# Kernel tuning notes

Hardware: AMD Instinct MI355X
Metric: run time of the kernel (lower is better)

## Reference

```python
import jax, jax.numpy as jnp
from jax import lax
import numpy as np

RANK = 4
C_IN = 32
C_OUT = 64
H, W = 128, 256
L1 = (H + 2, W + 2)      # conv k=3, pad=2, stride=1 -> H+2
L2 = (L1[0] + 2, L1[1] + 2)
EPS = 1e-5


def setup_inputs() -> dict:
    key = jax.random.key(0)
    ks = jax.random.split(key, 12)
    s = lambda k, shp: jax.random.normal(k, shp, dtype=jnp.float32) * 0.05
    inp = {
        "x": jax.random.normal(ks[0], (16, C_IN, H, W), dtype=jnp.float32),
        # layer 1: rank basis kernels, bias, outer combining-weight logits
        "w1": s(ks[1], (RANK, C_OUT, C_IN, 3, 3)),
        "b1": jnp.zeros((C_OUT,), jnp.float32),
        "a1h": s(ks[2], (RANK, L1[0])),
        "a1w": s(ks[3], (RANK, L1[1])),
        "g1": jnp.ones((C_OUT,), jnp.float32),
        "be1": jnp.zeros((C_OUT,), jnp.float32),
        # layer 2
        "w2": s(ks[4], (RANK, C_OUT, C_OUT, 3, 3)),
        "b2": jnp.zeros((C_OUT,), jnp.float32),
        "a2h": s(ks[5], (RANK, L2[0])),
        "a2w": s(ks[6], (RANK, L2[1])),
        "g2": jnp.ones((C_OUT,), jnp.float32),
        "be2": jnp.zeros((C_OUT,), jnp.float32),
    }
    return inp


def _combining_weights(ah, aw):
    # outer sum of row/col logits, softmax over rank -> [rank, Lh, Lw]
    return jax.nn.softmax(ah[:, :, None] + aw[:, None, :], axis=0)


def _lrlc(x, w, b, cw):
    # x: [B, Cin, H, W]; w: [rank, Cout, Cin, 3, 3]; cw: [rank, H', W']
    rank, co, ci, kh, kw = w.shape
    y = lax.conv_general_dilated(
        x, w.reshape(rank * co, ci, kh, kw),
        window_strides=(1, 1), padding=[(2, 2), (2, 2)],
        dimension_numbers=("NCHW", "OIHW", "NCHW"))
    B, _, Ho, Wo = y.shape
    y = y.reshape(B, rank, co, Ho, Wo)
    return jnp.einsum("brohw,rhw->bohw", y, cw) + b[None, :, None, None]


def _bn_relu(x, g, be):
    # training-mode BatchNorm2d (batch stats, biased variance) + ReLU
    mean = jnp.mean(x, axis=(0, 2, 3), keepdims=True)
    var = jnp.var(x, axis=(0, 2, 3), keepdims=True)
    xn = (x - mean) * lax.rsqrt(var + EPS)
    return jax.nn.relu(xn * g[None, :, None, None] + be[None, :, None, None])


def _maxpool3(x):
    return lax.reduce_window(x, -jnp.inf, lax.max,
                             (1, 1, 3, 3), (1, 1, 3, 3), "VALID")


def reference(x, w1, b1, a1h, a1w, g1, be1, w2, b2, a2h, a2w, g2, be2):
    cw1 = _combining_weights(a1h, a1w)
    h = _lrlc(x, w1, b1, cw1)
    h = _bn_relu(h, g1, be1)
    cw2 = _combining_weights(a2h, a2w)
    h = _lrlc(h, w2, b2, cw2)
    h = _bn_relu(h, g2, be2)
    return _maxpool3(h)
```

## Files before the change

kernel.cpp:

```cpp
#include <hip/hip_runtime.h>
#include <hip/hip_bf16.h>
#include <math.h>

#define COUT 64
#define EPS  1e-5f

typedef __hip_bfloat16 bf16;
typedef short  short8  __attribute__((ext_vector_type(8)));
typedef short  short4v __attribute__((ext_vector_type(4)));
typedef float  floatx4 __attribute__((ext_vector_type(4)));

__device__ __forceinline__ short bf16_bits(float f) {
    union { __hip_bfloat16 h; short s; } u;
    u.h = __float2bfloat16(f);
    return u.s;
}
__device__ __forceinline__ float bits_to_f32(short s) {
    union { __hip_bfloat16 h; short s; } u;
    u.s = s;
    return __bfloat162float(u.h);
}

#define NV1   33800
#define NV2   34584
#define XPAD_PLANE  (132*260)
#define H1_PLANE    (134*262)
#define H2_PLANE    (132*260)
#define NPOS1 (16*130*258)
#define NPOS2 (16*132*260)

__global__ void zero_f_kernel(float* __restrict__ p, int n) {
    int i = blockIdx.x*blockDim.x + threadIdx.x;
    if (i < n) p[i] = 0.f;
}
__global__ void zero4_kernel(uint4* __restrict__ p, long n4) {
    long i = (long)blockIdx.x*blockDim.x + threadIdx.x;
    for (; i < n4; i += (long)gridDim.x*blockDim.x) p[i] = make_uint4(0,0,0,0);
}

__global__ void cwv_kernel(const float* __restrict__ ah, const float* __restrict__ aw,
                           float* __restrict__ cwv, int Nv, int Wv, int Lh, int Lw) {
    int idx = blockIdx.x*blockDim.x + threadIdx.x;
    if (idx >= Nv) return;
    int oh = idx / Wv, ow = idx - oh*Wv;
    if (ow > Lw-1) ow = Lw-1;
    float v0 = ah[0*Lh+oh] + aw[0*Lw+ow];
    float v1 = ah[1*Lh+oh] + aw[1*Lw+ow];
    float v2 = ah[2*Lh+oh] + aw[2*Lw+ow];
    float v3 = ah[3*Lh+oh] + aw[3*Lw+ow];
    float m = fmaxf(fmaxf(v0,v1), fmaxf(v2,v3));
    v0 = __expf(v0-m); v1 = __expf(v1-m); v2 = __expf(v2-m); v3 = __expf(v3-m);
    float inv = 1.f/(v0+v1+v2+v3);
    cwv[0*(size_t)Nv+idx] = v0*inv; cwv[1*(size_t)Nv+idx] = v1*inv;
    cwv[2*(size_t)Nv+idx] = v2*inv; cwv[3*(size_t)Nv+idx] = v3*inv;
}

template<int CIN_, int NSLICES>
__global__ void pack_kernel(const float* __restrict__ w, short* __restrict__ Apk) {
    int gid = blockIdx.x*256 + threadIdx.x;
    if (gid >= NSLICES*1024) return;
    int l = gid & 63, t = (gid >> 6) & 15, s = gid >> 10;
    int m = t*16 + (l & 15);
    int r = m >> 6, co = m & 63;
    int kbase = s*32 + ((l >> 4) << 3);
    short8 v;
    #pragma unroll
    for (int j = 0; j < 8; ++j) {
        int k = kbase + j;
        int tap = k / CIN_, ci = k % CIN_;
        v[j] = bf16_bits(w[(((size_t)(r*COUT + co))*CIN_ + ci)*9 + tap]);
    }
    *reinterpret_cast<short8*>(Apk + (size_t)gid*8) = v;
}

__global__ void xpad_kernel(const float* __restrict__ x, short* __restrict__ xp) {
    int row = blockIdx.x;
    int b = row / 132, ih = row - b*132;
    int ci = threadIdx.x & 31, iw0 = threadIdx.x >> 5;
    for (int iw = iw0; iw < 260; iw += 8) {
        float v = 0.f;
        if (ih >= 2 && ih < 130 && iw >= 2 && iw < 258)
            v = x[(((size_t)b*32 + ci)*128 + (ih-2))*256 + (iw-2)];
        xp[((size_t)row*260 + iw)*32 + ci] = bf16_bits(v);
    }
}

template<int CIN_, int NSLICES>
__launch_bounds__(256, 2)
__global__ void lrlc_conv(const short* __restrict__ Bpl, const short* __restrict__ Apk,
                          const float* __restrict__ cwv, const float* __restrict__ bias,
                          short* __restrict__ Out, float* __restrict__ sum, float* __restrict__ sq,
                          int Wv, int Hout, int Wreal, int Nv, int inPlanePos,
                          int outW, int outPlanePos, int outPad) {
    const int tid  = threadIdx.x;
    const int w    = tid >> 6, l = tid & 63;
    const int quad = l >> 4, l15 = l & 15;
    const int b    = blockIdx.y;
    const int n0   = blockIdx.x * 128;

    __shared__ float cwS[4*128];
    for (int t = tid; t < 512; t += 256) {
        int r = t >> 7, nn = t & 127;
        int n = n0 + nn; if (n > Nv-1) n = Nv-1;
        cwS[t] = cwv[(size_t)r*Nv + n];
    }
    __syncthreads();

    const short* Bb = Bpl + (size_t)b*inPlanePos*CIN_;
    int bOff[8];
    #pragma unroll
    for (int j = 0; j < 8; ++j) bOff[j] = (n0 + j*16 + l15)*CIN_ + quad*8;
    const short* Aw = Apk + (size_t)(w*64 + l)*8;

    floatx4 acc[4][8];
    #pragma unroll
    for (int i = 0; i < 4; ++i)
        #pragma unroll
        for (int j = 0; j < 8; ++j)
            acc[i][j] = (floatx4){0.f,0.f,0.f,0.f};

    #pragma unroll
    for (int s = 0; s < NSLICES; ++s) {
        const int tap = (CIN_ == 32) ? s : (s >> 1);
        const int cb  = (CIN_ == 32) ? 0 : ((s & 1) << 5);
        const int koff = ((tap/3)*Wv + (tap%3))*CIN_ + cb;
        short8 bfr[8], afr[4];
        #pragma unroll
        for (int j = 0; j < 8; ++j)
            bfr[j] = *reinterpret_cast<const short8*>(Bb + bOff[j] + koff);
        #pragma unroll
        for (int i = 0; i < 4; ++i)
            afr[i] = *reinterpret_cast<const short8*>(Aw + (size_t)(s*16 + i*4)*512);
        #pragma unroll
        for (int i = 0; i < 4; ++i)
            #pragma unroll
            for (int j = 0; j < 8; ++j)
                acc[i][j] = __builtin_amdgcn_mfma_f32_16x16x32_bf16(afr[i], bfr[j], acc[i][j], 0, 0, 0);
    }

    const int co_base = w*16 + quad*4;
    float bs[4];
    #pragma unroll
    for (int rg = 0; rg < 4; ++rg) bs[rg] = bias[co_base + rg];
    float st[4] = {0.f,0.f,0.f,0.f}, st2[4] = {0.f,0.f,0.f,0.f};
    #pragma unroll
    for (int j = 0; j < 8; ++j) {
        int nl = j*16 + l15;
        int n  = n0 + nl;
        int oh = n / Wv, ow = n - oh*Wv;
        bool valid = (ow < Wreal) && (oh < Hout);
        float c0 = cwS[nl], c1 = cwS[128+nl], c2 = cwS[256+nl], c3 = cwS[384+nl];
        short4v pk;
        #pragma unroll
        for (int rg = 0; rg < 4; ++rg) {
            float v = acc[0][j][rg]*c0 + acc[1][j][rg]*c1
                    + acc[2][j][rg]*c2 + acc[3][j][rg]*c3 + bs[rg];
            if (valid) { st[rg] += v; st2[rg] = fmaf(v, v, st2[rg]); }
            pk[rg] = bf16_bits(v);
        }
        if (valid) {
            size_t op = ((size_t)b*outPlanePos + (size_t)(oh + outPad)*outW + (ow + outPad))*(size_t)COUT + co_base;
            *reinterpret_cast<short4v*>(Out + op) = pk;
        }
    }
    #pragma unroll
    for (int m = 1; m < 16; m <<= 1) {
        #pragma unroll
        for (int rg = 0; rg < 4; ++rg) {
            st[rg]  += __shfl_xor(st[rg],  m, 16);
            st2[rg] += __shfl_xor(st2[rg], m, 16);
        }
    }
    if (l15 == 0) {
        #pragma unroll
        for (int rg = 0; rg < 4; ++rg) {
            atomicAdd(&sum[co_base+rg], st[rg]);
            atomicAdd(&sq[co_base+rg],  st2[rg]);
        }
    }
}

__global__ void finalize_kernel(const float* __restrict__ sum, const float* __restrict__ sumsq,
                                const float* __restrict__ g, const float* __restrict__ be,
                                float* __restrict__ A, float* __restrict__ Bc, float cnt) {
    int c = threadIdx.x;
    if (c >= COUT) return;
    float mean = sum[c]/cnt;
    float var  = sumsq[c]/cnt - mean*mean;
    float inv  = rsqrtf(var + EPS);
    float a = g[c]*inv;
    A[c]  = a;
    Bc[c] = fmaf(-mean, a, be[c]);
}

__global__ void bnrelu_rows(short* __restrict__ h, const float* __restrict__ A,
                            const float* __restrict__ Bc) {
    __shared__ float sA[64], sB[64];
    if (threadIdx.x < 64) { sA[threadIdx.x] = A[threadIdx.x]; sB[threadIdx.x] = Bc[threadIdx.x]; }
    __syncthreads();
    int row = blockIdx.x;
    int b = row / 130, oh = row - b*130;
    short* base = h + ((size_t)(b*134 + oh + 2)*262 + 2)*64;
    const int nvec = 258*64/8;
    for (int it = threadIdx.x; it < nvec; it += 256) {
        short8 d = *reinterpret_cast<short8*>(base + it*8);
        int c0 = (it*8) & 63;
        #pragma unroll
        for (int q = 0; q < 8; ++q) {
            float v = bits_to_f32(d[q]);
            int c = c0 + q;
            v = fmaxf(fmaf(v, sA[c], sB[c]), 0.f);
            d[q] = bf16_bits(v);
        }
        *reinterpret_cast<short8*>(base + it*8) = d;
    }
}

__global__ void maxpool_rows(const short* __restrict__ h2, const float* __restrict__ A,
                             const float* __restrict__ Bc, float* __restrict__ out) {
    __shared__ float sA[64], sB[64];
    if (threadIdx.x < 64) { sA[threadIdx.x] = A[threadIdx.x]; sB[threadIdx.x] = Bc[threadIdx.x]; }
    __syncthreads();
    int row = blockIdx.x;
    int b = row / 44, ph = row - b*44;
    for (int item = threadIdx.x; item < 86*16; item += 256) {
        int cg = item & 15, pw = item >> 4;
        float m[4] = {0.f,0.f,0.f,0.f};
        #pragma unroll
        for (int i = 0; i < 3; ++i) {
            const short* rp = h2 + ((size_t)(b*132 + ph*3 + i)*260 + pw*3)*64 + cg*4;
            #pragma unroll
            for (int j = 0; j < 3; ++j) {
                short4v d = *reinterpret_cast<const short4v*>(rp + j*64);
                #pragma unroll
                for (int q = 0; q < 4; ++q) {
                    int c = cg*4 + q;
                    float v = fmaf(bits_to_f32(d[q]), sA[c], sB[c]);
                    m[q] = fmaxf(m[q], v);
                }
            }
        }
        #pragma unroll
        for (int q = 0; q < 4; ++q)
            out[((size_t)(b*64 + cg*4 + q)*44 + ph)*86 + pw] = m[q];
    }
}

extern "C" void kernel_launch(void* const* d_in, const int* in_sizes, int n_in,
                              void* d_out, int out_size, void* d_ws, size_t ws_size,
                              hipStream_t stream) {
    const float* x   = (const float*)d_in[0];
    const float* w1  = (const float*)d_in[1];
    const float* b1  = (const float*)d_in[2];
    const float* a1h = (const float*)d_in[3];
    const float* a1w = (const float*)d_in[4];
    const float* g1  = (const float*)d_in[5];
    const float* be1 = (const float*)d_in[6];
    const float* w2  = (const float*)d_in[7];
    const float* b2  = (const float*)d_in[8];
    const float* a2h = (const float*)d_in[9];
    const float* a2w = (const float*)d_in[10];
    const float* g2  = (const float*)d_in[11];
    const float* be2 = (const float*)d_in[12];
    float* out = (float*)d_out;

    char* ws = (char*)d_ws;
    float* stats = (float*)ws;
    float* sum1 = stats;       float* sq1 = stats + 64;
    float* A1   = stats + 128; float* Bc1 = stats + 192;
    float* sum2 = stats + 256; float* sq2 = stats + 320;
    float* A2   = stats + 384; float* Bc2 = stats + 448;
    float* cw1v = (float*)(ws + 2048);
    float* cw2v = cw1v + 4*NV1;
    short* Apk1 = (short*)(cw2v + 4*NV2);
    short* Apk2 = Apk1 + 73728;
    short* h1pad = Apk2 + 147456;
    short* xpad  = h1pad + (size_t)16*H1_PLANE*64 + 4096;
    short* h2    = xpad;

    zero_f_kernel<<<2, 256, 0, stream>>>(stats, 512);
    {
        long n4 = ((size_t)16*H1_PLANE*64 + 4096) * 2 / 16;
        zero4_kernel<<<4096, 256, 0, stream>>>((uint4*)h1pad, n4);
    }
    cwv_kernel<<<(NV1+255)/256, 256, 0, stream>>>(a1h, a1w, cw1v, NV1, 260, 130, 258);
    cwv_kernel<<<(NV2+255)/256, 256, 0, stream>>>(a2h, a2w, cw2v, NV2, 262, 132, 260);
    pack_kernel<32, 9><<<(9*1024+255)/256, 256, 0, stream>>>(w1, Apk1);
    pack_kernel<64,18><<<(18*1024+255)/256, 256, 0, stream>>>(w2, Apk2);
    xpad_kernel<<<16*132, 256, 0, stream>>>(x, xpad);

    lrlc_conv<32, 9><<<dim3((NV1+127)/128, 16), 256, 0, stream>>>(
        xpad, Apk1, cw1v, b1, h1pad, sum1, sq1,
        260, 130, 258, NV1, XPAD_PLANE, 262, H1_PLANE, 2);
    finalize_kernel<<<1, 64, 0, stream>>>(sum1, sq1, g1, be1, A1, Bc1, (float)NPOS1);
    bnrelu_rows<<<16*130, 256, 0, stream>>>(h1pad, A1, Bc1);

    lrlc_conv<64,18><<<dim3((NV2+127)/128, 16), 256, 0, stream>>>(
        h1pad, Apk2, cw2v, b2, h2, sum2, sq2,
        262, 132, 260, NV2, H1_PLANE, 260, H2_PLANE, 0);
    finalize_kernel<<<1, 64, 0, stream>>>(sum2, sq2, g2, be2, A2, Bc2, (float)NPOS2);

    maxpool_rows<<<16*44, 256, 0, stream>>>(h2, A2, Bc2, out);
}
```

Measured before the change: 1.186 ms.

## Merge prep kernels, zero only h1pad borders, halve conv tile, prefetch A fragments

Combines the stats-zeroing, softmax combining-weight, and weight-packing launches into one prep kernel. Replaces the full zero-fill of the padded h1 buffer with a kernel that zeroes only its border ring, fused with the input padding/transposition. The conv tile shrinks from 128 to 64 positions per block, cutting accumulator registers and doubling the grid, and the A fragments for the next slice are double-buffered and loaded early. The smaller tile lowers B-operand reuse per A load in exchange for higher occupancy and fewer launches.

Result: slower. 1.945 ms (+64.0%).

```diff
diff --git a/kernel.cpp b/kernel.cpp
--- a/kernel.cpp
+++ b/kernel.cpp
@@ -28,22 +28,21 @@
 #define H2_PLANE    (132*260)
 #define NPOS1 (16*130*258)
 #define NPOS2 (16*132*260)
-
-__global__ void zero_f_kernel(float* __restrict__ p, int n) {
-    int i = blockIdx.x*blockDim.x + threadIdx.x;
-    if (i < n) p[i] = 0.f;
-}
-__global__ void zero4_kernel(uint4* __restrict__ p, long n4) {
-    long i = (long)blockIdx.x*blockDim.x + threadIdx.x;
-    for (; i < n4; i += (long)gridDim.x*blockDim.x) p[i] = make_uint4(0,0,0,0);
-}
-
-__global__ void cwv_kernel(const float* __restrict__ ah, const float* __restrict__ aw,
-                           float* __restrict__ cwv, int Nv, int Wv, int Lh, int Lw) {
-    int idx = blockIdx.x*blockDim.x + threadIdx.x;
+#define CW1_N (130*258)
+#define CW2_N (132*260)
+
+#define CW1_BLK ((CW1_N + 255)/256)
+#define CW2_BLK ((CW2_N + 255)/256)
+#define PK1_BLK (9*1024/256)
+#define PK2_BLK (18*1024/256)
+
+__device__ __forceinline__ void cwv_body(const float* __restrict__ ah, const float* __restrict__ aw,
+                                         float* __restrict__ cwv, int Nv, int Wv,
+                                         int Lh, int Lw, int idx) {
     if (idx >= Nv) return;
     int oh = idx / Wv, ow = idx - oh*Wv;
     if (ow > Lw-1) ow = Lw-1;
+    if (oh > Lh-1) oh = Lh-1;
     float v0 = ah[0*Lh+oh] + aw[0*Lw+ow];
     float v1 = ah[1*Lh+oh] + aw[1*Lw+ow];
     float v2 = ah[2*Lh+oh] + aw[2*Lw+ow];
@@ -54,10 +53,11 @@
     cwv[0*(size_t)Nv+idx] = v0*inv; cwv[1*(size_t)Nv+idx] = v1*inv;
     cwv[2*(size_t)Nv+idx] = v2*inv; cwv[3*(size_t)Nv+idx] = v3*inv;
 }
+#define CWV1_BLK ((NV1 + 255)/256)
+#define CWV2_BLK ((NV2 + 255)/256)
 
 template<int CIN_, int NSLICES>
-__global__ void pack_kernel(const float* __restrict__ w, short* __restrict__ Apk) {
-    int gid = blockIdx.x*256 + threadIdx.x;
+__device__ __forceinline__ void pack_body(const float* __restrict__ w, short* __restrict__ Apk, int gid) {
     if (gid >= NSLICES*1024) return;
     int l = gid & 63, t = (gid >> 6) & 15, s = gid >> 10;
     int m = t*16 + (l & 15);
@@ -73,15 +73,55 @@
     *reinterpret_cast<short8*>(Apk + (size_t)gid*8) = v;
 }
 
-__global__ void xpad_kernel(const float* __restrict__ x, short* __restrict__ xp) {
-    int row = blockIdx.x;
-    int b = row / 132, ih = row - b*132;
-    int ci = threadIdx.x & 31, iw0 = threadIdx.x >> 5;
-    for (int iw = iw0; iw < 260; iw += 8) {
-        float v = 0.f;
-        if (ih >= 2 && ih < 130 && iw >= 2 && iw < 258)
-            v = x[(((size_t)b*32 + ci)*128 + (ih-2))*256 + (iw-2)];
-        xp[((size_t)row*260 + iw)*32 + ci] = bf16_bits(v);
+__global__ void prep_kernel(const float* __restrict__ a1h, const float* __restrict__ a1w,
+                            const float* __restrict__ a2h, const float* __restrict__ a2w,
+                            const float* __restrict__ w1, const float* __restrict__ w2,
+                            float* __restrict__ stats, float* __restrict__ cwv1,
+                            float* __restrict__ cwv2, short* __restrict__ Apk1,
+                            short* __restrict__ Apk2) {
+    int bx = blockIdx.x;
+    if (bx == 0) {
+        stats[threadIdx.x] = 0.f; stats[threadIdx.x + 256] = 0.f;
+    } else if (bx < 1 + CWV1_BLK) {
+        cwv_body(a1h, a1w, cwv1, NV1, 260, 130, 258, (bx-1)*256 + threadIdx.x);
+    } else if (bx < 1 + CWV1_BLK + CWV2_BLK) {
+        cwv_body(a2h, a2w, cwv2, NV2, 262, 132, 260, (bx-(1+CWV1_BLK))*256 + threadIdx.x);
+    } else if (bx < 1 + CWV1_BLK + CWV2_BLK + PK1_BLK) {
+        pack_body<32, 9>(w1, Apk1, (bx-(1+CWV1_BLK+CWV2_BLK))*256 + threadIdx.x);
+    } else {
+        pack_body<64,18>(w2, Apk2, (bx-(1+CWV1_BLK+CWV2_BLK+PK1_BLK))*256 + threadIdx.x);
+    }
+}
+#define PREP_BLOCKS (1 + CWV1_BLK + CWV2_BLK + PK1_BLK + PK2_BLK)
+
+__global__ void border_xpad_kernel(short* __restrict__ h1p,
+                                   const float* __restrict__ x, short* __restrict__ xp) {
+    if (blockIdx.x < 16) {
+        int b = blockIdx.x;
+        short* base = h1p + (size_t)b*H1_PLANE*64;
+        short8 z = (short8){0,0,0,0,0,0,0,0};
+        for (int it = threadIdx.x; it < 4*262*8; it += 256) {
+            int pos = it >> 3, g = it & 7;
+            int rr = pos / 262, cc = pos - rr*262;
+            int row = (rr < 2) ? rr : 130 + rr;
+            *reinterpret_cast<short8*>(base + ((size_t)row*262 + cc)*64 + g*8) = z;
+        }
+        for (int it = threadIdx.x; it < 130*4*8; it += 256) {
+            int pos = it >> 3, g = it & 7;
+            int rr = pos >> 2, k = pos & 3;
+            int col = (k < 2) ? k : 258 + k;
+            *reinterpret_cast<short8*>(base + ((size_t)(rr+2)*262 + col)*64 + g*8) = z;
+        }
+    } else {
+        int row = blockIdx.x - 16;
+        int b = row / 132, ih = row - b*132;
+        int ci = threadIdx.x & 31, iw0 = threadIdx.x >> 5;
+        for (int iw = iw0; iw < 260; iw += 8) {
+            float v = 0.f;
+            if (ih >= 2 && ih < 130 && iw >= 2 && iw < 258)
+                v = x[(((size_t)b*32 + ci)*128 + (ih-2))*256 + (iw-2)];
+            xp[((size_t)row*260 + iw)*32 + ci] = bf16_bits(v);
+        }
     }
 }
 
@@ -96,46 +136,53 @@
     const int w    = tid >> 6, l = tid & 63;
     const int quad = l >> 4, l15 = l & 15;
     const int b    = blockIdx.y;
-    const int n0   = blockIdx.x * 128;
-
-    __shared__ float cwS[4*128];
-    for (int t = tid; t < 512; t += 256) {
-        int r = t >> 7, nn = t & 127;
+    const int n0   = blockIdx.x * 64;
+
+    __shared__ float cwS[256];
+    {
+        int r = tid >> 6, nn = tid & 63;
         int n = n0 + nn; if (n > Nv-1) n = Nv-1;
-        cwS[t] = cwv[(size_t)r*Nv + n];
+        cwS[r*64 + nn] = cwv[(size_t)r*Nv + n];
     }
     __syncthreads();
 
     const short* Bb = Bpl + (size_t)b*inPlanePos*CIN_;
-    int bOff[8];
-    #pragma unroll
-    for (int j = 0; j < 8; ++j) bOff[j] = (n0 + j*16 + l15)*CIN_ + quad*8;
+    int bOff[4];
+    #pragma unroll
+    for (int j = 0; j < 4; ++j) bOff[j] = (n0 + j*16 + l15)*CIN_ + quad*8;
     const short* Aw = Apk + (size_t)(w*64 + l)*8;
 
-    floatx4 acc[4][8];
+    floatx4 acc[4][4];
     #pragma unroll
     for (int i = 0; i < 4; ++i)
         #pragma unroll
-        for (int j = 0; j < 8; ++j)
+        for (int j = 0; j < 4; ++j)
             acc[i][j] = (floatx4){0.f,0.f,0.f,0.f};
 
+    auto loadA = [&](int s, short8* afr) {
+        #pragma unroll
+        for (int i = 0; i < 4; ++i)
+            afr[i] = *reinterpret_cast<const short8*>(Aw + (size_t)(s*16 + i*4)*512);
+    };
+    short8 afr[2][4];
+    loadA(0, afr[0]);
+
     #pragma unroll
     for (int s = 0; s < NSLICES; ++s) {
+        const int cur = s & 1;
         const int tap = (CIN_ == 32) ? s : (s >> 1);
         const int cb  = (CIN_ == 32) ? 0 : ((s & 1) << 5);
         const int koff = ((tap/3)*Wv + (tap%3))*CIN_ + cb;
-        short8 bfr[8], afr[4];
-        #pragma unroll
-        for (int j = 0; j < 8; ++j)
+        short8 bfr[4];
+        #pragma unroll
+        for (int j = 0; j < 4; ++j)
             bfr[j] = *reinterpret_cast<const short8*>(Bb + bOff[j] + koff);
-        #pragma unroll
-        for (int i = 0; i < 4; ++i)
-            afr[i] = *reinterpret_cast<const short8*>(Aw + (size_t)(s*16 + i*4)*512);
+        if (s + 1 < NSLICES) loadA(s+1, afr[cur ^ 1]);
         #pragma unroll
         for (int i = 0; i < 4; ++i)
             #pragma unroll
-            for (int j = 0; j < 8; ++j)
-                acc[i][j] = __builtin_amdgcn_mfma_f32_16x16x32_bf16(afr[i], bfr[j], acc[i][j], 0, 0, 0);
+            for (int j = 0; j < 4; ++j)
+                acc[i][j] = __builtin_amdgcn_mfma_f32_16x16x32_bf16(afr[cur][i], bfr[j], acc[i][j], 0, 0, 0);
     }
 
     const int co_base = w*16 + quad*4;
@@ -144,12 +191,12 @@
     for (int rg = 0; rg < 4; ++rg) bs[rg] = bias[co_base + rg];
     float st[4] = {0.f,0.f,0.f,0.f}, st2[4] = {0.f,0.f,0.f,0.f};
     #pragma unroll
-    for (int j = 0; j < 8; ++j) {
+    for (int j = 0; j < 4; ++j) {
         int nl = j*16 + l15;
         int n  = n0 + nl;
         int oh = n / Wv, ow = n - oh*Wv;
         bool valid = (ow < Wreal) && (oh < Hout);
-        float c0 = cwS[nl], c1 = cwS[128+nl], c2 = cwS[256+nl], c3 = cwS[384+nl];
+        float c0 = cwS[nl], c1 = cwS[64+nl], c2 = cwS[128+nl], c3 = cwS[192+nl];
         short4v pk;
         #pragma unroll
         for (int rg = 0; rg < 4; ++rg) {
@@ -270,34 +317,29 @@
     float* A1   = stats + 128; float* Bc1 = stats + 192;
     float* sum2 = stats + 256; float* sq2 = stats + 320;
     float* A2   = stats + 384; float* Bc2 = stats + 448;
-    float* cw1v = (float*)(ws + 2048);
-    float* cw2v = cw1v + 4*NV1;
-    short* Apk1 = (short*)(cw2v + 4*NV2);
+    float* cwv1 = (float*)(ws + 2048);
+    float* cwv2 = cwv1 + 4*NV1;
+    short* Apk1 = (short*)(cwv2 + 4*NV2);
     short* Apk2 = Apk1 + 73728;
     short* h1pad = Apk2 + 147456;
     short* xpad  = h1pad + (size_t)16*H1_PLANE*64 + 4096;
     short* h2    = xpad;
 
-    zero_f_kernel<<<2, 256, 0, stream>>>(stats, 512);
-    {
-        long n4 = ((size_t)16*H1_PLANE*64 + 4096) * 2 / 16;
-        zero4_kernel<<<4096, 256, 0, stream>>>((uint4*)h1pad, n4);
-    }
-    cwv_kernel<<<(NV1+255)/256, 256, 0, stream>>>(a1h, a1w, cw1v, NV1, 260, 130, 258);
-    cwv_kernel<<<(NV2+255)/256, 256, 0, stream>>>(a2h, a2w, cw2v, NV2, 262, 132, 260);
-    pack_kernel<32, 9><<<(9*1024+255)/256, 256, 0, stream>>>(w1, Apk1);
-    pack_kernel<64,18><<<(18*1024+255)/256, 256, 0, stream>>>(w2, Apk2);
-    xpad_kernel<<<16*132, 256, 0, stream>>>(x, xpad);
-
-    lrlc_conv<32, 9><<<dim3((NV1+127)/128, 16), 256, 0, stream>>>(
-        xpad, Apk1, cw1v, b1, h1pad, sum1, sq1,
-        260, 130, 258, NV1, XPAD_PLANE, 262, H1_PLANE, 2);
+    prep_kernel<<<PREP_BLOCKS, 256, 0, stream>>>(a1h, a1w, a2h, a2w, w1, w2,
+                                                 stats, cwv1, cwv2, Apk1, Apk2);
+    border_xpad_kernel<<<16 + 16*132, 256, 0, stream>>>(h1pad, x, xpad);
+
+    lrlc_conv<32, 9><<<dim3((NV1+63)/64, 16), 256, 0, stream>>>(
+        xpad, Apk1, cwv1, b1, h1pad, sum1, sq1,
+        260, 130, 258, NV1, XPAD_PLANE,
+        262, H1_PLANE, 2);
     finalize_kernel<<<1, 64, 0, stream>>>(sum1, sq1, g1, be1, A1, Bc1, (float)NPOS1);
     bnrelu_rows<<<16*130, 256, 0, stream>>>(h1pad, A1, Bc1);
 
-    lrlc_conv<64,18><<<dim3((NV2+127)/128, 16), 256, 0, stream>>>(
-        h1pad, Apk2, cw2v, b2, h2, sum2, sq2,
-        262, 132, 260, NV2, H1_PLANE, 260, H2_PLANE, 0);
+    lrlc_conv<64,18><<<dim3((NV2+63)/64, 16), 256, 0, stream>>>(
+        h1pad, Apk2, cwv2, b2, h2, sum2, sq2,
+        262, 132, 260, NV2, H1_PLANE,
+        260, H2_PLANE, 0);
     finalize_kernel<<<1, 64, 0, stream>>>(sum2, sq2, g2, be2, A2, Bc2, (float)NPOS2);
 
     maxpool_rows<<<16*44, 256, 0, stream>>>(h2, A2, Bc2, out);
```
